# Optimization experiments

Hardware: AMD Instinct MI355X
Metric: run time of the kernel (lower is better)

The kernel has to match this reference:

```python
import jax, jax.numpy as jnp
import numpy as np

B, S, D, H, M, E, K = 4, 2048, 1024, 2048, 64, 8, 2  # batch, seq, d_model, max_neurons, moe_hidden, experts, top_k


def setup_inputs() -> dict:
    key = jax.random.key(0)
    ks = jax.random.split(key, 10)
    r = lambda k, shape: jax.random.normal(k, shape, dtype=jnp.float32) * 0.02
    return {
        "inputs_embeds": jax.random.normal(ks[0], (B, S, D), dtype=jnp.float32),
        "enc_W": r(ks[1], (D, H)), "enc_b": jnp.zeros((H,), jnp.float32),
        "s2c_W": r(ks[2], (H, M)), "s2c_b": jnp.zeros((M,), jnp.float32),
        "rW1": r(ks[3], (M, 64)), "rb1": jnp.zeros((64,), jnp.float32),
        "rW2": r(ks[4], (64, E)), "rb2": jnp.zeros((E,), jnp.float32),
        "We1": r(ks[5], (E, M, H // 2)), "be1": jnp.zeros((E, H // 2), jnp.float32),
        "We2": r(ks[6], (E, H // 2, M)), "be2": jnp.zeros((E, M), jnp.float32),
        "c2s_W": r(ks[7], (M, H)), "c2s_b": jnp.zeros((H,), jnp.float32),
        "dec_W": r(ks[8], (H, D)), "dec_b": jnp.zeros((D,), jnp.float32),
        "ln_g": jnp.ones((D,), jnp.float32), "ln_b": jnp.zeros((D,), jnp.float32),
    }


def _layernorm(x, g, b, eps=1e-5):
    mu = x.mean(-1, keepdims=True)
    var = ((x - mu) ** 2).mean(-1, keepdims=True)
    return (x - mu) * jax.lax.rsqrt(var + eps) * g + b


def _forward(inputs_embeds, enc_W, enc_b, s2c_W, s2c_b, rW1, rb1, rW2, rb2,
             We1, be1, We2, be2, c2s_W, c2s_b, dec_W, dec_b, ln_g, ln_b):
    b, s, _ = inputs_embeds.shape
    # GIFNeuron encoder (rate-coded surrogate spikes)
    spikes_enc = jax.nn.sigmoid(inputs_embeds @ enc_W + enc_b)          # (B,S,H)
    flat = spikes_enc.reshape(b * s, H)                                  # (N,H)
    # SpikeToContinuousBridge ('rate'): projection to MoE hidden
    cont = flat @ s2c_W + s2c_b                                          # (N,M)
    # LiquidMoERouter: 2-layer router, softmax, top-k, renormalize
    logits = jnp.tanh(cont @ rW1 + rb1) @ rW2 + rb2                      # (N,E)
    probs = jax.nn.softmax(logits, axis=-1)
    topw, topi = jax.lax.top_k(probs, K)                                 # (N,K)
    w = topw / topw.sum(-1, keepdims=True)
    # dense per-token per-expert gate == sum_k weights[:,k] * (indices[:,k]==e)
    gates = (jax.nn.one_hot(topi, E, dtype=cont.dtype) * w[..., None]).sum(1)  # (N,E)
    # SNNExpert MLP per expert, dense dispatch + weighted combine (index_add equivalent)
    h = jax.nn.relu(jnp.einsum('nm,emh->enh', cont, We1) + be1[:, None, :])    # (E,N,H/2)
    expert_out = jnp.einsum('enh,ehm->enm', h, We2) + be2[:, None, :]          # (E,N,M)
    output_flat = jnp.einsum('enm,ne->nm', expert_out, gates)                  # (N,M)
    # ContinuousToSpikeBridge ('poisson', expected rate), 2D -> 1 timestep
    spikes_moe = jax.nn.sigmoid(output_flat @ c2s_W + c2s_b).reshape(b, s, H)
    # GIFNeuron decoder + LayerNorm
    decoded = jax.nn.sigmoid(spikes_moe @ dec_W + dec_b)                 # (B,S,D)
    return _layernorm(decoded, ln_g, ln_b)


def reference(inputs_embeds, enc_W, enc_b, s2c_W, s2c_b, rW1, rb1, rW2, rb2,
              We1, be1, We2, be2, c2s_W, c2s_b, dec_W, dec_b, ln_g, ln_b):
    return _forward(inputs_embeds, enc_W, enc_b, s2c_W, s2c_b, rW1, rb1, rW2, rb2,
                    We1, be1, We2, be2, c2s_W, c2s_b, dec_W, dec_b, ln_g, ln_b)
```

## Files before the change

### kernel.cpp

```cpp
#include <hip/hip_runtime.h>
#include <hip/hip_bf16.h>
#include <cstdint>
#include <cstddef>

#define TOK    8192
#define DMODEL 1024
#define HDIM   2048
#define MDIM   64
#define NEXP   8
#define HHALF  1024

using f32x4  = __attribute__((ext_vector_type(4))) float;
using bf16x8 = __attribute__((ext_vector_type(8))) __bf16;
using bf16x4 = __attribute__((ext_vector_type(4))) __bf16;

__device__ __forceinline__ void async16(const void* g, void* l) {
  __builtin_amdgcn_global_load_lds(
      (const __attribute__((address_space(1))) unsigned int*)g,
      (__attribute__((address_space(3))) unsigned int*)l, 16, 0, 0);
}

__global__ __launch_bounds__(256) void preamble_kernel(
    const float* __restrict__ X, __bf16* __restrict__ Xb,
    const float* __restrict__ encW, __bf16* __restrict__ encWT,
    const float* __restrict__ s2cW, __bf16* __restrict__ s2cWT,
    const float* __restrict__ c2sW, __bf16* __restrict__ c2sWT,
    const float* __restrict__ decW, __bf16* __restrict__ decWT,
    const float* __restrict__ We1, __bf16* __restrict__ We1T,
    const float* __restrict__ We2, __bf16* __restrict__ We2T) {
  __shared__ float ts[32][33];
  const int tid = threadIdx.x;
  int b = blockIdx.x;
  if (b < 8192) {
    int i = b * 256 + tid;
    float4 v = ((const float4*)X)[i];
    bf16x4 o = { (__bf16)v.x, (__bf16)v.y, (__bf16)v.z, (__bf16)v.w };
    ((bf16x4*)Xb)[i] = o;
    return;
  }
  b -= 8192;
  const float* in; __bf16* outp; int R, C, tx, ty;
  if (b < 2048)              { in = encW; outp = encWT; R = 1024; C = 2048; tx = b % 64; ty = b / 64; }
  else if ((b -= 2048) < 128){ in = s2cW; outp = s2cWT; R = 2048; C = 64;   tx = b % 2;  ty = b / 2;  }
  else if ((b -= 128) < 128) { in = c2sW; outp = c2sWT; R = 64;   C = 2048; tx = b % 64; ty = b / 64; }
  else if ((b -= 128) < 2048){ in = decW; outp = decWT; R = 2048; C = 1024; tx = b % 32; ty = b / 32; }
  else if ((b -= 2048) < 512){ int s = b / 64, t = b % 64;
                               in = We1 + (size_t)s * 65536; outp = We1T + (size_t)s * 65536;
                               R = 64; C = 1024; tx = t % 32; ty = t / 32; }
  else                       { b -= 512; int s = b / 64, t = b % 64;
                               in = We2 + (size_t)s * 65536; outp = We2T + (size_t)s * 65536;
                               R = 1024; C = 64; tx = t % 2; ty = t / 2; }
  const int c0 = tx * 32, r0 = ty * 32;
  const int x = tid & 31, y = tid >> 5;
  #pragma unroll
  for (int i = y; i < 32; i += 8) ts[i][x] = in[(size_t)(r0 + i) * C + c0 + x];
  __syncthreads();
  #pragma unroll
  for (int i = y; i < 32; i += 8)
    outp[(size_t)(c0 + i) * R + r0 + x] = (__bf16)ts[x][i];
}
#define PREAMBLE_BLOCKS (8192 + 2048 + 128 + 128 + 2048 + 512 + 512)

template <int BN, int WAVES, int NBUF, int OUT_BF16, int ACT, int BIAS>
__global__ __launch_bounds__(WAVES * 64, WAVES == 8 ? 2 : 1) void gemm_mt(
    const __bf16* __restrict__ A, const __bf16* __restrict__ Bt,
    const float* __restrict__ bias, void* __restrict__ Cout,
    int M, int N, int K) {
  constexpr int BM = 256, BK = 64;
  constexpr int A_ISSUES = BM / (8 * WAVES);
  constexpr int B_ISSUES = BN / (8 * WAVES);
  constexpr int LOADS = A_ISSUES + B_ISSUES;
  static_assert((NBUF == 2 && LOADS == 8) || (NBUF == 3 && LOADS == 12),
                "vmcnt literals assume LOADS=8 (NBUF2) or 12 (NBUF3)");
  __shared__ __bf16 As[NBUF * BM * BK];
  __shared__ __bf16 Bs[NBUF * BN * BK];
  const int tid = threadIdx.x;
  const int wave = tid >> 6, lane = tid & 63;
  const int quad = lane >> 4, l16 = lane & 15;
  const int m0 = blockIdx.x * BM, n0 = blockIdx.y * BN;
  const int wm = (wave & 1) * 128;
  const int wn = (wave >> 1) * 64;
  const int lrow = lane >> 3, lchunk = lane & 7;
  f32x4 acc[8][4] = {};

  const __bf16* aSrc[A_ISSUES];
  const __bf16* bSrc[B_ISSUES];
  #pragma unroll
  for (int t = 0; t < A_ISSUES; ++t) {
    int row = (t * WAVES + wave) * 8 + lrow;
    aSrc[t] = A + (size_t)(m0 + row) * K + (lchunk ^ (row & 7)) * 8;
  }
  #pragma unroll
  for (int t = 0; t < B_ISSUES; ++t) {
    int row = (t * WAVES + wave) * 8 + lrow;
    bSrc[t] = Bt + (size_t)(n0 + row) * K + (lchunk ^ (row & 7)) * 8;
  }
  int aOff[8], bOff[4];
  #pragma unroll
  for (int rf = 0; rf < 8; ++rf) {
    int row = wm + rf * 16 + l16;
    aOff[rf] = row * BK + ((quad ^ (row & 7)) * 8);
  }
  #pragma unroll
  for (int cf = 0; cf < 4; ++cf) {
    int row = wn + cf * 16 + l16;
    bOff[cf] = row * BK + ((quad ^ (row & 7)) * 8);
  }

  auto stage = [&](__bf16* Ad, __bf16* Bd) {
    #pragma unroll
    for (int t = 0; t < A_ISSUES; ++t) {
      async16(aSrc[t], Ad + (t * WAVES + wave) * 8 * BK);
      aSrc[t] += BK;
    }
    #pragma unroll
    for (int t = 0; t < B_ISSUES; ++t) {
      async16(bSrc[t], Bd + (t * WAVES + wave) * 8 * BK);
      bSrc[t] += BK;
    }
  };

  __bf16 *cA0 = As, *cA1 = As + BM * BK, *cA2 = As + 2 * BM * BK;
  __bf16 *cB0 = Bs, *cB1 = Bs + BN * BK, *cB2 = Bs + 2 * BN * BK;
  const int nt = K / BK;
  stage(cA0, cB0);
  if constexpr (NBUF == 3) stage(cA1, cB1);

  for (int t = 0; t < nt; ++t) {
    if constexpr (NBUF == 2) {
      if (t + 1 < nt) stage(cA1, cB1);
    } else {
      if (t + 2 < nt) stage(cA2, cB2);
    }
    const int ahead = nt - 1 - t;
    if constexpr (NBUF == 2) {
      if (ahead >= 1) asm volatile("s_waitcnt vmcnt(8)" ::: "memory");
      else            asm volatile("s_waitcnt vmcnt(0)" ::: "memory");
    } else {
      if (ahead >= 2)      asm volatile("s_waitcnt vmcnt(24)" ::: "memory");
      else if (ahead == 1) asm volatile("s_waitcnt vmcnt(12)" ::: "memory");
      else                 asm volatile("s_waitcnt vmcnt(0)" ::: "memory");
    }
    asm volatile("s_barrier" ::: "memory");

    bf16x8 af[4], ag[4], bv[4], bw[4];
    #pragma unroll
    for (int r = 0; r < 4; ++r) af[r] = *(const bf16x8*)(cA0 + aOff[r]);
    #pragma unroll
    for (int c = 0; c < 4; ++c) bv[c] = *(const bf16x8*)(cB0 + bOff[c]);
    #pragma unroll
    for (int r = 0; r < 4; ++r) ag[r] = *(const bf16x8*)(cA0 + aOff[4 + r]);
    __builtin_amdgcn_s_setprio(1);
    #pragma unroll
    for (int c = 0; c < 4; ++c)
      #pragma unroll
      for (int r = 0; r < 4; ++r)
        acc[r][c] = __builtin_amdgcn_mfma_f32_16x16x32_bf16(af[r], bv[c], acc[r][c], 0, 0, 0);
    __builtin_amdgcn_s_setprio(0);
    asm volatile("s_barrier" ::: "memory");
    #pragma unroll
    for (int r = 0; r < 4; ++r) af[r] = *(const bf16x8*)(cA0 + (aOff[r] ^ 32));
    #pragma unroll
    for (int c = 0; c < 4; ++c) bw[c] = *(const bf16x8*)(cB0 + (bOff[c] ^ 32));
    __builtin_amdgcn_s_setprio(1);
    #pragma unroll
    for (int c = 0; c < 4; ++c)
      #pragma unroll
      for (int r = 0; r < 4; ++r)
        acc[4 + r][c] = __builtin_amdgcn_mfma_f32_16x16x32_bf16(ag[r], bv[c], acc[4 + r][c], 0, 0, 0);
    __builtin_amdgcn_s_setprio(0);
    asm volatile("s_barrier" ::: "memory");
    #pragma unroll
    for (int r = 0; r < 4; ++r) ag[r] = *(const bf16x8*)(cA0 + (aOff[4 + r] ^ 32));
    __builtin_amdgcn_s_setprio(1);
    #pragma unroll
    for (int c = 0; c < 4; ++c)
      #pragma unroll
      for (int r = 0; r < 4; ++r)
        acc[r][c] = __builtin_amdgcn_mfma_f32_16x16x32_bf16(af[r], bw[c], acc[r][c], 0, 0, 0);
    __builtin_amdgcn_s_setprio(0);
    asm volatile("s_barrier" ::: "memory");
    __builtin_amdgcn_s_setprio(1);
    #pragma unroll
    for (int c = 0; c < 4; ++c)
      #pragma unroll
      for (int r = 0; r < 4; ++r)
        acc[4 + r][c] = __builtin_amdgcn_mfma_f32_16x16x32_bf16(ag[r], bw[c], acc[4 + r][c], 0, 0, 0);
    __builtin_amdgcn_s_setprio(0);
    asm volatile("s_barrier" ::: "memory");

    if constexpr (NBUF == 2) {
      __bf16* x;
      x = cA0; cA0 = cA1; cA1 = x;
      x = cB0; cB0 = cB1; cB1 = x;
    } else {
      __bf16* x;
      x = cA0; cA0 = cA1; cA1 = cA2; cA2 = x;
      x = cB0; cB0 = cB1; cB1 = cB2; cB2 = x;
    }
  }

  #pragma unroll
  for (int rf = 0; rf < 8; ++rf)
    #pragma unroll
    for (int cf = 0; cf < 4; ++cf)
      #pragma unroll
      for (int r = 0; r < 4; ++r) {
        int m = m0 + wm + rf * 16 + quad * 4 + r;
        int n = n0 + wn + cf * 16 + l16;
        float v = acc[rf][cf][r];
        if (BIAS) v += bias[n];
        if (ACT == 1) v = 1.0f / (1.0f + __expf(-v));
        if (OUT_BF16)
          ((__bf16*)Cout)[(size_t)m * N + n] = (__bf16)v;
        else
          ((float*)Cout)[(size_t)m * N + n] = v;
      }
}

template <int BM, int BN, int WAVES, int OUT_BF16, int ACT, int BIAS, int SUMA>
__global__ __launch_bounds__(WAVES * 64) void gemm_bt(
    const __bf16* __restrict__ A, const __bf16* __restrict__ Bt,
    const float* __restrict__ bias, void* __restrict__ Cout,
    int M, int N, int K, const __bf16* __restrict__ A2) {
  constexpr int BK = 64;
  constexpr int WAVES_N = WAVES / 2;
  constexpr int WTM = BM / 32;
  constexpr int WTN = BN / (WAVES_N * 16);
  constexpr int NBUF = SUMA ? 1 : 3;
  constexpr int A_ISSUES = BM / (8 * WAVES);
  constexpr int B_ISSUES = BN / (8 * WAVES);
  static_assert(SUMA || (A_ISSUES + B_ISSUES == 6), "vmcnt literal assumes 6 loads/stage");
  __shared__ __bf16 As[NBUF * BM * BK];
  __shared__ __bf16 Bs[NBUF * BN * BK];
  const int tid = threadIdx.x;
  const int wave = tid >> 6, lane = tid & 63;
  const int quad = lane >> 4, l16 = lane & 15;
  const int m0 = blockIdx.x * BM, n0 = blockIdx.y * BN;
  const int ks = K / gridDim.z;
  const int kbeg = blockIdx.z * ks;
  const int wm = (wave & 1) * (BM / 2);
  const int wn = (wave >> 1) * (BN / WAVES_N);
  const int lrow = lane >> 3;
  const int lchunk = lane & 7;
  f32x4 acc[WTM][WTN] = {};

  const __bf16* aSrc[A_ISSUES];
  const __bf16* bSrc[B_ISSUES];
  #pragma unroll
  for (int t = 0; t < A_ISSUES; ++t) {
    int row = (t * WAVES + wave) * 8 + lrow;
    aSrc[t] = A + (size_t)(m0 + row) * K + kbeg + (lchunk ^ (row & 7)) * 8;
  }
  #pragma unroll
  for (int t = 0; t < B_ISSUES; ++t) {
    int row = (t * WAVES + wave) * 8 + lrow;
    bSrc[t] = Bt + (size_t)(n0 + row) * K + kbeg + (lchunk ^ (row & 7)) * 8;
  }
  int aOff[WTM][2], bOff[WTN][2];
  #pragma unroll
  for (int i = 0; i < WTM; ++i) {
    int row = wm + i * 16 + l16;
    #pragma unroll
    for (int kk = 0; kk < 2; ++kk)
      aOff[i][kk] = row * BK + (((kk * 4 + quad) ^ (row & 7)) * 8);
  }
  #pragma unroll
  for (int j = 0; j < WTN; ++j) {
    int row = wn + j * 16 + l16;
    #pragma unroll
    for (int kk = 0; kk < 2; ++kk)
      bOff[j][kk] = row * BK + (((kk * 4 + quad) ^ (row & 7)) * 8);
  }

  auto stage = [&](__bf16* Ad, __bf16* Bd) {
    #pragma unroll
    for (int t = 0; t < A_ISSUES; ++t) {
      async16(aSrc[t], Ad + (t * WAVES + wave) * 8 * BK);
      aSrc[t] += BK;
    }
    #pragma unroll
    for (int t = 0; t < B_ISSUES; ++t) {
      async16(bSrc[t], Bd + (t * WAVES + wave) * 8 * BK);
      bSrc[t] += BK;
    }
  };
  auto compute = [&](const __bf16* Ab, const __bf16* Bb) {
    #pragma unroll
    for (int kk = 0; kk < 2; ++kk) {
      bf16x8 af[WTM], bfr[WTN];
      #pragma unroll
      for (int i = 0; i < WTM; ++i) af[i] = *(const bf16x8*)(Ab + aOff[i][kk]);
      #pragma unroll
      for (int j = 0; j < WTN; ++j) bfr[j] = *(const bf16x8*)(Bb + bOff[j][kk]);
      #pragma unroll
      for (int i = 0; i < WTM; ++i)
        #pragma unroll
        for (int j = 0; j < WTN; ++j)
          acc[i][j] = __builtin_amdgcn_mfma_f32_16x16x32_bf16(af[i], bfr[j], acc[i][j], 0, 0, 0);
    }
  };

  const int niter = ks / BK;
  if constexpr (SUMA) {
    for (int it = 0; it < niter; ++it) {
      __syncthreads();
      #pragma unroll
      for (int t = 0; t < A_ISSUES; ++t) {
        int row = (t * WAVES + wave) * 8 + lrow;
        size_t go = (size_t)(m0 + row) * K + kbeg + it * BK + lchunk * 8;
        bf16x8 a0 = *(const bf16x8*)(A + go);
        bf16x8 a1 = *(const bf16x8*)(A2 + go);
        bf16x8 s;
        #pragma unroll
        for (int q = 0; q < 8; ++q) s[q] = (__bf16)((float)a0[q] + (float)a1[q]);
        *(bf16x8*)(As + row * BK + ((lchunk ^ (row & 7)) * 8)) = s;
      }
      #pragma unroll
      for (int t = 0; t < B_ISSUES; ++t) {
        async16(bSrc[t], Bs + (t * WAVES + wave) * 8 * BK);
        bSrc[t] += BK;
      }
      __syncthreads();
      compute(As, Bs);
    }
  } else {
    __bf16* a0 = As;  __bf16* a1 = As + BM * BK;  __bf16* a2 = As + 2 * BM * BK;
    __bf16* b0 = Bs;  __bf16* b1 = Bs + BN * BK;  __bf16* b2 = Bs + 2 * BN * BK;
    stage(a0, b0);
    if (niter > 1) stage(a1, b1);
    for (int it = 0; it < niter; ++it) {
      if (it + 1 < niter) asm volatile("s_waitcnt vmcnt(6)" ::: "memory");
      else                asm volatile("s_waitcnt vmcnt(0)" ::: "memory");
      __builtin_amdgcn_s_barrier();
      if (it + 2 < niter) stage(a2, b2);
      compute(a0, b0);
      __bf16* t;
      t = a0; a0 = a1; a1 = a2; a2 = t;
      t = b0; b0 = b1; b1 = b2; b2 = t;
    }
  }

  char* Cz = (char*)Cout + (size_t)blockIdx.z * M * N * (OUT_BF16 ? 2 : 4);
  #pragma unroll
  for (int i = 0; i < WTM; ++i)
    #pragma unroll
    for (int j = 0; j < WTN; ++j)
      #pragma unroll
      for (int r = 0; r < 4; ++r) {
        int m = m0 + wm + i * 16 + quad * 4 + r;
        int n = n0 + wn + j * 16 + l16;
        float v = acc[i][j][r];
        if (BIAS) v += bias[n];
        if (ACT == 1) v = 1.0f / (1.0f + __expf(-v));
        if (OUT_BF16)
          ((__bf16*)Cz)[(size_t)m * N + n] = (__bf16)v;
        else
          ((float*)Cz)[(size_t)m * N + n] = v;
      }
}

__global__ __launch_bounds__(256) void router_kernel(
    const float* __restrict__ contP, const float* __restrict__ s2c_b,
    const float* __restrict__ rW1, const float* __restrict__ rb1,
    const float* __restrict__ rW2, const float* __restrict__ rb2,
    __bf16* __restrict__ contB, int* __restrict__ e01,
    float2* __restrict__ g01) {
  const int wave = threadIdx.x >> 6, lane = threadIdx.x & 63;
  const int n = blockIdx.x * 4 + wave;
  const size_t base = (size_t)n * 64 + lane;
  const size_t slab = (size_t)TOK * 64;
  float c = contP[base] + contP[base + slab] + contP[base + 2 * slab] +
            contP[base + 3 * slab] + s2c_b[lane];
  contB[base] = (__bf16)c;
  float acc = rb1[lane];
  #pragma unroll
  for (int i = 0; i < 64; ++i) {
    float ci = __shfl(c, i);
    acc = fmaf(ci, rW1[i * 64 + lane], acc);
  }
  float t = tanhf(acc);
  float logit[8];
  #pragma unroll
  for (int e = 0; e < 8; ++e) {
    float v = t * rW2[lane * 8 + e];
    #pragma unroll
    for (int o = 32; o; o >>= 1) v += __shfl_xor(v, o);
    logit[e] = v + rb2[e];
  }
  float mx = logit[0];
  #pragma unroll
  for (int e = 1; e < 8; ++e) mx = fmaxf(mx, logit[e]);
  float p[8];
  #pragma unroll
  for (int e = 0; e < 8; ++e) p[e] = __expf(logit[e] - mx);
  float v0 = p[0]; int e0 = 0;
  #pragma unroll
  for (int e = 1; e < 8; ++e) if (p[e] > v0) { v0 = p[e]; e0 = e; }
  float v1 = -1.0f; int e1 = 0;
  #pragma unroll
  for (int e = 0; e < 8; ++e) if (e != e0 && p[e] > v1) { v1 = p[e]; e1 = e; }
  float inv = 1.0f / (v0 + v1);
  if (lane == 0) {
    e01[n] = e0 | (e1 << 8);
    g01[n] = make_float2(v0 * inv, v1 * inv);
  }
}

__global__ __launch_bounds__(256) void moe_fused_kernel(
    const __bf16* __restrict__ contB, const __bf16* __restrict__ We1T,
    const __bf16* __restrict__ We2T, const float* __restrict__ be1,
    const float* __restrict__ be2, const int* __restrict__ e01,
    const float2* __restrict__ g01, __bf16* __restrict__ slab0,
    __bf16* __restrict__ slab1) {
  constexpr int TT = 128;
  const int e = blockIdx.y;
  const int t0 = blockIdx.x * TT;
  __shared__ __bf16 cont_s[TT * 64];
  __shared__ __bf16 w1_s[64 * 64];
  __shared__ __bf16 w2_s[64 * 64];
  __shared__ __bf16 h_s[TT * 64];
  __shared__ int   e01_s[TT];
  __shared__ float g0_s[TT], g1_s[TT];
  const int tid = threadIdx.x;
  const int wave = tid >> 6, lane = tid & 63;
  const int quad = lane >> 4, l16 = lane & 15;
  if (tid < TT) {
    e01_s[tid] = e01[t0 + tid];
    float2 g = g01[t0 + tid];
    g0_s[tid] = g.x; g1_s[tid] = g.y;
  }
  for (int i = tid; i < TT * 8; i += 256) {
    int r = i >> 3, cc = i & 7;
    *(uint4*)(cont_s + r * 64 + ((cc ^ (r & 7)) * 8)) =
        *(const uint4*)(contB + (size_t)(t0 + r) * 64 + cc * 8);
  }
  const int wtok = wave * 32;
  f32x4 acc2[2][4] = {};
  for (int hc = 0; hc < HHALF; hc += 64) {
    __syncthreads();
    for (int c = tid; c < 512; c += 256) {
      int r = c >> 3, cc = c & 7;
      *(uint4*)(w1_s + r * 64 + ((cc ^ (r & 7)) * 8)) =
          *(const uint4*)(We1T + ((size_t)e * HHALF + hc + r) * 64 + cc * 8);
      *(uint4*)(w2_s + r * 64 + ((cc ^ (r & 7)) * 8)) =
          *(const uint4*)(We2T + ((size_t)e * 64 + r) * HHALF + hc + cc * 8);
    }
    __syncthreads();
    f32x4 acc1[2][4] = {};
    #pragma unroll
    for (int kk = 0; kk < 2; ++kk) {
      bf16x8 af[2], bfr[4];
      #pragma unroll
      for (int i = 0; i < 2; ++i) {
        int row = wtok + i * 16 + l16;
        af[i] = *(const bf16x8*)(cont_s + row * 64 + (((kk * 4 + quad) ^ (row & 7)) * 8));
      }
      #pragma unroll
      for (int j = 0; j < 4; ++j) {
        int row = j * 16 + l16;
        bfr[j] = *(const bf16x8*)(w1_s + row * 64 + (((kk * 4 + quad) ^ (row & 7)) * 8));
      }
      #pragma unroll
      for (int i = 0; i < 2; ++i)
        #pragma unroll
        for (int j = 0; j < 4; ++j)
          acc1[i][j] = __builtin_amdgcn_mfma_f32_16x16x32_bf16(af[i], bfr[j], acc1[i][j], 0, 0, 0);
    }
    #pragma unroll
    for (int i = 0; i < 2; ++i)
      #pragma unroll
      for (int j = 0; j < 4; ++j)
        #pragma unroll
        for (int r = 0; r < 4; ++r) {
          int tr = wtok + i * 16 + quad * 4 + r;
          int hcol = j * 16 + l16;
          float v = acc1[i][j][r] + be1[e * HHALF + hc + hcol];
          h_s[tr * 64 + (((hcol >> 3) ^ (tr & 7)) * 8) + (hcol & 7)] =
              (__bf16)fmaxf(v, 0.0f);
        }
    #pragma unroll
    for (int kk = 0; kk < 2; ++kk) {
      bf16x8 af[2], bfr[4];
      #pragma unroll
      for (int i = 0; i < 2; ++i) {
        int row = wtok + i * 16 + l16;
        af[i] = *(const bf16x8*)(h_s + row * 64 + (((kk * 4 + quad) ^ (row & 7)) * 8));
      }
      #pragma unroll
      for (int j = 0; j < 4; ++j) {
        int row = j * 16 + l16;
        bfr[j] = *(const bf16x8*)(w2_s + row * 64 + (((kk * 4 + quad) ^ (row & 7)) * 8));
      }
      #pragma unroll
      for (int i = 0; i < 2; ++i)
        #pragma unroll
        for (int j = 0; j < 4; ++j)
          acc2[i][j] = __builtin_amdgcn_mfma_f32_16x16x32_bf16(af[i], bfr[j], acc2[i][j], 0, 0, 0);
    }
  }
  #pragma unroll
  for (int i = 0; i < 2; ++i)
    #pragma unroll
    for (int j = 0; j < 4; ++j)
      #pragma unroll
      for (int r = 0; r < 4; ++r) {
        int tr = wtok + i * 16 + quad * 4 + r;
        int m = j * 16 + l16;
        int pe = e01_s[tr];
        size_t o = (size_t)(t0 + tr) * 64 + m;
        if ((pe & 0xff) == e)
          slab0[o] = (__bf16)(g0_s[tr] * (acc2[i][j][r] + be2[e * 64 + m]));
        else if (((pe >> 8) & 0xff) == e)
          slab1[o] = (__bf16)(g1_s[tr] * (acc2[i][j][r] + be2[e * 64 + m]));
      }
}

__global__ __launch_bounds__(256) void ln_kernel(
    const float* __restrict__ x, const float* __restrict__ g,
    const float* __restrict__ b, float* __restrict__ out) {
  const int row = blockIdx.x;
  const float4 v = ((const float4*)(x + (size_t)row * 1024))[threadIdx.x];
  float s1 = v.x + v.y + v.z + v.w;
  float s2 = v.x * v.x + v.y * v.y + v.z * v.z + v.w * v.w;
  #pragma unroll
  for (int o = 32; o; o >>= 1) { s1 += __shfl_xor(s1, o); s2 += __shfl_xor(s2, o); }
  __shared__ float ws1[4], ws2[4];
  const int wave = threadIdx.x >> 6, lane = threadIdx.x & 63;
  if (lane == 0) { ws1[wave] = s1; ws2[wave] = s2; }
  __syncthreads();
  s1 = ws1[0] + ws1[1] + ws1[2] + ws1[3];
  s2 = ws2[0] + ws2[1] + ws2[2] + ws2[3];
  const float mu = s1 * (1.0f / 1024.0f);
  const float var = s2 * (1.0f / 1024.0f) - mu * mu;
  const float inv = rsqrtf(var + 1e-5f);
  const int col = threadIdx.x * 4;
  const float4 gv = *(const float4*)(g + col);
  const float4 bv = *(const float4*)(b + col);
  float4 o;
  o.x = (v.x - mu) * inv * gv.x + bv.x;
  o.y = (v.y - mu) * inv * gv.y + bv.y;
  o.z = (v.z - mu) * inv * gv.z + bv.z;
  o.w = (v.w - mu) * inv * gv.w + bv.w;
  *(float4*)(out + (size_t)row * 1024 + col) = o;
}

extern "C" void kernel_launch(void* const* d_in, const int* in_sizes, int n_in,
                              void* d_out, int out_size, void* d_ws, size_t ws_size,
                              hipStream_t stream) {
  const float* X     = (const float*)d_in[0];
  const float* enc_W = (const float*)d_in[1];
  const float* enc_b = (const float*)d_in[2];
  const float* s2c_W = (const float*)d_in[3];
  const float* s2c_b = (const float*)d_in[4];
  const float* rW1   = (const float*)d_in[5];
  const float* rb1   = (const float*)d_in[6];
  const float* rW2   = (const float*)d_in[7];
  const float* rb2   = (const float*)d_in[8];
  const float* We1   = (const float*)d_in[9];
  const float* be1   = (const float*)d_in[10];
  const float* We2   = (const float*)d_in[11];
  const float* be2   = (const float*)d_in[12];
  const float* c2s_W = (const float*)d_in[13];
  const float* c2s_b = (const float*)d_in[14];
  const float* dec_W = (const float*)d_in[15];
  const float* dec_b = (const float*)d_in[16];
  const float* ln_g  = (const float*)d_in[17];
  const float* ln_b  = (const float*)d_in[18];
  float* out = (float*)d_out;

  char* ws = (char*)d_ws;
  size_t off = 0;
  auto take = [&](size_t bytes) -> char* {
    char* p = ws + off;
    off = (off + bytes + 255) & ~(size_t)255;
    return p;
  };
  const size_t SLAB = (size_t)TOK * HDIM * 2;
  char*   slabA     = take(SLAB);
  char*   slabB     = take(SLAB);
  __bf16* encWT     = (__bf16*)take((size_t)HDIM * DMODEL * 2);
  __bf16* s2cWT     = (__bf16*)take((size_t)MDIM * HDIM * 2);
  __bf16* c2sWT     = (__bf16*)take((size_t)HDIM * MDIM * 2);
  __bf16* decWT     = (__bf16*)take((size_t)DMODEL * HDIM * 2);
  __bf16* We1T      = (__bf16*)take((size_t)NEXP * HHALF * MDIM * 2);
  __bf16* We2T      = (__bf16*)take((size_t)NEXP * MDIM * HHALF * 2);
  __bf16* contB     = (__bf16*)take((size_t)TOK * MDIM * 2);
  int*    e01       = (int*)take((size_t)TOK * 4);
  float2* g01       = (float2*)take((size_t)TOK * 8);
  __bf16* oslab0    = (__bf16*)take((size_t)TOK * MDIM * 2);
  __bf16* oslab1    = (__bf16*)take((size_t)TOK * MDIM * 2);
  if (off > ws_size) return;

  __bf16* Xb        = (__bf16*)slabA;
  float*  contP     = (float*)(slabA + (size_t)TOK * DMODEL * 2);
  __bf16* spikesMoe = (__bf16*)slabA;
  __bf16* spikesEnc = (__bf16*)slabB;
  float*  decoded   = (float*)slabB;

  preamble_kernel<<<PREAMBLE_BLOCKS, 256, 0, stream>>>(
      X, Xb, enc_W, encWT, s2c_W, s2cWT, c2s_W, c2sWT, dec_W, decWT,
      We1, We1T, We2, We2T);

  gemm_mt<256, 8, 2, 1, 1, 1><<<dim3(TOK / 256, HDIM / 256), 512, 0, stream>>>(
      Xb, encWT, enc_b, spikesEnc, TOK, HDIM, DMODEL);
  gemm_bt<128, 64, 4, 0, 0, 0, 0><<<dim3(TOK / 128, 1, 4), 256, 0, stream>>>(
      spikesEnc, s2cWT, nullptr, contP, TOK, MDIM, HDIM, nullptr);
  router_kernel<<<TOK / 4, 256, 0, stream>>>(contP, s2c_b, rW1, rb1, rW2, rb2,
                                             contB, e01, g01);
  moe_fused_kernel<<<dim3(TOK / 128, NEXP), 256, 0, stream>>>(
      contB, We1T, We2T, be1, be2, e01, g01, oslab0, oslab1);
  gemm_bt<128, 128, 4, 1, 1, 1, 1><<<dim3(TOK / 128, HDIM / 128, 1), 256, 0, stream>>>(
      oslab0, c2sWT, c2s_b, spikesMoe, TOK, HDIM, MDIM, oslab1);
  gemm_mt<128, 4, 3, 0, 1, 1><<<dim3(TOK / 256, DMODEL / 128), 256, 0, stream>>>(
      spikesMoe, decWT, dec_b, decoded, TOK, DMODEL, HDIM);
  ln_kernel<<<TOK, 256, 0, stream>>>(decoded, ln_g, ln_b, out);
}
```

Before: 320.3 us.

## Switch MoE to sparse top-k dispatch and rework GEMM pipelining

New measurement: 311.7 us. -2.7%, faster.

```diff
diff --git a/kernel.cpp b/kernel.cpp
--- a/kernel.cpp
+++ b/kernel.cpp
@@ -62,7 +62,7 @@
 #define PREAMBLE_BLOCKS (8192 + 2048 + 128 + 128 + 2048 + 512 + 512)
 
 template <int BN, int WAVES, int NBUF, int OUT_BF16, int ACT, int BIAS>
-__global__ __launch_bounds__(WAVES * 64, WAVES == 8 ? 2 : 1) void gemm_mt(
+__global__ __launch_bounds__(WAVES * 64, 2) void gemm_mt(
     const __bf16* __restrict__ A, const __bf16* __restrict__ Bt,
     const float* __restrict__ bias, void* __restrict__ Cout,
     int M, int N, int K) {
@@ -70,8 +70,7 @@
   constexpr int A_ISSUES = BM / (8 * WAVES);
   constexpr int B_ISSUES = BN / (8 * WAVES);
   constexpr int LOADS = A_ISSUES + B_ISSUES;
-  static_assert((NBUF == 2 && LOADS == 8) || (NBUF == 3 && LOADS == 12),
-                "vmcnt literals assume LOADS=8 (NBUF2) or 12 (NBUF3)");
+  static_assert(NBUF == 2 && LOADS == 8, "vmcnt literal assumes LOADS=8");
   __shared__ __bf16 As[NBUF * BM * BK];
   __shared__ __bf16 Bs[NBUF * BN * BK];
   const int tid = threadIdx.x;
@@ -120,27 +119,15 @@
     }
   };
 
-  __bf16 *cA0 = As, *cA1 = As + BM * BK, *cA2 = As + 2 * BM * BK;
-  __bf16 *cB0 = Bs, *cB1 = Bs + BN * BK, *cB2 = Bs + 2 * BN * BK;
+  __bf16 *cA0 = As, *cA1 = As + BM * BK;
+  __bf16 *cB0 = Bs, *cB1 = Bs + BN * BK;
   const int nt = K / BK;
   stage(cA0, cB0);
-  if constexpr (NBUF == 3) stage(cA1, cB1);
 
   for (int t = 0; t < nt; ++t) {
-    if constexpr (NBUF == 2) {
-      if (t + 1 < nt) stage(cA1, cB1);
-    } else {
-      if (t + 2 < nt) stage(cA2, cB2);
-    }
-    const int ahead = nt - 1 - t;
-    if constexpr (NBUF == 2) {
-      if (ahead >= 1) asm volatile("s_waitcnt vmcnt(8)" ::: "memory");
-      else            asm volatile("s_waitcnt vmcnt(0)" ::: "memory");
-    } else {
-      if (ahead >= 2)      asm volatile("s_waitcnt vmcnt(24)" ::: "memory");
-      else if (ahead == 1) asm volatile("s_waitcnt vmcnt(12)" ::: "memory");
-      else                 asm volatile("s_waitcnt vmcnt(0)" ::: "memory");
-    }
+    if (t + 1 < nt) stage(cA1, cB1);
+    if (t + 1 < nt) asm volatile("s_waitcnt vmcnt(8)" ::: "memory");
+    else            asm volatile("s_waitcnt vmcnt(0)" ::: "memory");
     asm volatile("s_barrier" ::: "memory");
 
     bf16x8 af[4], ag[4], bv[4], bw[4];
@@ -189,15 +176,9 @@
     __builtin_amdgcn_s_setprio(0);
     asm volatile("s_barrier" ::: "memory");
 
-    if constexpr (NBUF == 2) {
-      __bf16* x;
-      x = cA0; cA0 = cA1; cA1 = x;
-      x = cB0; cB0 = cB1; cB1 = x;
-    } else {
-      __bf16* x;
-      x = cA0; cA0 = cA1; cA1 = cA2; cA2 = x;
-      x = cB0; cB0 = cB1; cB1 = cB2; cB2 = x;
-    }
+    __bf16* x;
+    x = cA0; cA0 = cA1; cA1 = x;
+    x = cB0; cB0 = cB1; cB1 = x;
   }
 
   #pragma unroll
@@ -227,10 +208,9 @@
   constexpr int WAVES_N = WAVES / 2;
   constexpr int WTM = BM / 32;
   constexpr int WTN = BN / (WAVES_N * 16);
-  constexpr int NBUF = SUMA ? 1 : 3;
+  constexpr int NBUF = SUMA ? 1 : 2;
   constexpr int A_ISSUES = BM / (8 * WAVES);
   constexpr int B_ISSUES = BN / (8 * WAVES);
-  static_assert(SUMA || (A_ISSUES + B_ISSUES == 6), "vmcnt literal assumes 6 loads/stage");
   __shared__ __bf16 As[NBUF * BM * BK];
   __shared__ __bf16 Bs[NBUF * BN * BK];
   const int tid = threadIdx.x;
@@ -325,20 +305,20 @@
       compute(As, Bs);
     }
   } else {
-    __bf16* a0 = As;  __bf16* a1 = As + BM * BK;  __bf16* a2 = As + 2 * BM * BK;
-    __bf16* b0 = Bs;  __bf16* b1 = Bs + BN * BK;  __bf16* b2 = Bs + 2 * BN * BK;
-    stage(a0, b0);
-    if (niter > 1) stage(a1, b1);
-    for (int it = 0; it < niter; ++it) {
-      if (it + 1 < niter) asm volatile("s_waitcnt vmcnt(6)" ::: "memory");
-      else                asm volatile("s_waitcnt vmcnt(0)" ::: "memory");
+    __bf16* curA = As;  __bf16* nxtA = As + BM * BK;
+    __bf16* curB = Bs;  __bf16* nxtB = Bs + BN * BK;
+    stage(curA, curB);
+    asm volatile("s_waitcnt vmcnt(0)" ::: "memory");
+    __builtin_amdgcn_s_barrier();
+    for (int it = 0; it < niter - 1; ++it) {
+      stage(nxtA, nxtB);
+      compute(curA, curB);
+      asm volatile("s_waitcnt vmcnt(0)" ::: "memory");
       __builtin_amdgcn_s_barrier();
-      if (it + 2 < niter) stage(a2, b2);
-      compute(a0, b0);
-      __bf16* t;
-      t = a0; a0 = a1; a1 = a2; a2 = t;
-      t = b0; b0 = b1; b1 = b2; b2 = t;
-    }
+      { __bf16* t = curA; curA = nxtA; nxtA = t; }
+      { __bf16* t = curB; curB = nxtB; nxtB = t; }
+    }
+    compute(curA, curB);
   }
 
   char* Cz = (char*)Cout + (size_t)blockIdx.z * M * N * (OUT_BF16 ? 2 : 4);
@@ -365,7 +345,8 @@
     const float* __restrict__ rW1, const float* __restrict__ rb1,
     const float* __restrict__ rW2, const float* __restrict__ rb2,
     __bf16* __restrict__ contB, int* __restrict__ e01,
-    float2* __restrict__ g01) {
+    float2* __restrict__ g01, int* __restrict__ cnt) {
+  if (blockIdx.x == 0 && threadIdx.x < NEXP) cnt[threadIdx.x] = 0;
   const int wave = threadIdx.x >> 6, lane = threadIdx.x & 63;
   const int n = blockIdx.x * 4 + wave;
   const size_t base = (size_t)n * 64 + lane;
@@ -407,36 +388,62 @@
   }
 }
 
-__global__ __launch_bounds__(256) void moe_fused_kernel(
+__global__ __launch_bounds__(256) void fill_kernel(
+    const int* __restrict__ e01, int* __restrict__ cnt,
+    unsigned* __restrict__ idxb) {
+  __shared__ int lcnt[NEXP], lbase[NEXP];
+  const int tid = threadIdx.x;
+  if (tid < NEXP) lcnt[tid] = 0;
+  __syncthreads();
+  const int n = blockIdx.x * 256 + tid;
+  const int pe = e01[n];
+  const int e0 = pe & 0xff, e1 = (pe >> 8) & 0xff;
+  const int p0 = atomicAdd(&lcnt[e0], 1);
+  const int p1 = atomicAdd(&lcnt[e1], 1);
+  __syncthreads();
+  if (tid < NEXP) lbase[tid] = atomicAdd(&cnt[tid], lcnt[tid]);
+  __syncthreads();
+  idxb[e0 * TOK + lbase[e0] + p0] = (unsigned)n;
+  idxb[e1 * TOK + lbase[e1] + p1] = (unsigned)n | 0x80000000u;
+}
+
+__global__ __launch_bounds__(256) void moe_sparse_kernel(
     const __bf16* __restrict__ contB, const __bf16* __restrict__ We1T,
     const __bf16* __restrict__ We2T, const float* __restrict__ be1,
-    const float* __restrict__ be2, const int* __restrict__ e01,
-    const float2* __restrict__ g01, __bf16* __restrict__ slab0,
-    __bf16* __restrict__ slab1) {
-  constexpr int TT = 128;
+    const float* __restrict__ be2, const unsigned* __restrict__ idxb,
+    const int* __restrict__ cnt, const float2* __restrict__ g01,
+    __bf16* __restrict__ slab0, __bf16* __restrict__ slab1) {
+  constexpr int TT = 64;
   const int e = blockIdx.y;
-  const int t0 = blockIdx.x * TT;
+  const int start = blockIdx.x * TT;
+  const int ne = cnt[e];
+  if (start >= ne) return;
+  const int nval = min(TT, ne - start);
   __shared__ __bf16 cont_s[TT * 64];
   __shared__ __bf16 w1_s[64 * 64];
   __shared__ __bf16 w2_s[64 * 64];
   __shared__ __bf16 h_s[TT * 64];
-  __shared__ int   e01_s[TT];
-  __shared__ float g0_s[TT], g1_s[TT];
+  __shared__ unsigned tok_s[TT];
+  __shared__ float gate_s[TT];
   const int tid = threadIdx.x;
   const int wave = tid >> 6, lane = tid & 63;
   const int quad = lane >> 4, l16 = lane & 15;
   if (tid < TT) {
-    e01_s[tid] = e01[t0 + tid];
-    float2 g = g01[t0 + tid];
-    g0_s[tid] = g.x; g1_s[tid] = g.y;
-  }
+    unsigned v = idxb[e * TOK + start + ((tid < nval) ? tid : 0)];
+    unsigned tok = v & 0x7fffffffu;
+    float2 g = g01[tok];
+    tok_s[tid] = v;
+    gate_s[tid] = (v >> 31) ? g.y : g.x;
+  }
+  __syncthreads();
   for (int i = tid; i < TT * 8; i += 256) {
     int r = i >> 3, cc = i & 7;
+    unsigned tok = tok_s[r] & 0x7fffffffu;
     *(uint4*)(cont_s + r * 64 + ((cc ^ (r & 7)) * 8)) =
-        *(const uint4*)(contB + (size_t)(t0 + r) * 64 + cc * 8);
-  }
-  const int wtok = wave * 32;
-  f32x4 acc2[2][4] = {};
+        *(const uint4*)(contB + (size_t)tok * 64 + cc * 8);
+  }
+  const int wtok = wave * 16;
+  f32x4 acc2[4] = {};
   for (int hc = 0; hc < HHALF; hc += 64) {
     __syncthreads();
     for (int c = tid; c < 512; c += 256) {
@@ -447,14 +454,13 @@
           *(const uint4*)(We2T + ((size_t)e * 64 + r) * HHALF + hc + cc * 8);
     }
     __syncthreads();
-    f32x4 acc1[2][4] = {};
+    f32x4 acc1[4] = {};
     #pragma unroll
     for (int kk = 0; kk < 2; ++kk) {
-      bf16x8 af[2], bfr[4];
-      #pragma unroll
-      for (int i = 0; i < 2; ++i) {
-        int row = wtok + i * 16 + l16;
-        af[i] = *(const bf16x8*)(cont_s + row * 64 + (((kk * 4 + quad) ^ (row & 7)) * 8));
+      bf16x8 af, bfr[4];
+      {
+        int row = wtok + l16;
+        af = *(const bf16x8*)(cont_s + row * 64 + (((kk * 4 + quad) ^ (row & 7)) * 8));
       }
       #pragma unroll
       for (int j = 0; j < 4; ++j) {
@@ -462,30 +468,25 @@
         bfr[j] = *(const bf16x8*)(w1_s + row * 64 + (((kk * 4 + quad) ^ (row & 7)) * 8));
       }
       #pragma unroll
-      for (int i = 0; i < 2; ++i)
-        #pragma unroll
-        for (int j = 0; j < 4; ++j)
-          acc1[i][j] = __builtin_amdgcn_mfma_f32_16x16x32_bf16(af[i], bfr[j], acc1[i][j], 0, 0, 0);
-    }
-    #pragma unroll
-    for (int i = 0; i < 2; ++i)
-      #pragma unroll
       for (int j = 0; j < 4; ++j)
-        #pragma unroll
-        for (int r = 0; r < 4; ++r) {
-          int tr = wtok + i * 16 + quad * 4 + r;
-          int hcol = j * 16 + l16;
-          float v = acc1[i][j][r] + be1[e * HHALF + hc + hcol];
-          h_s[tr * 64 + (((hcol >> 3) ^ (tr & 7)) * 8) + (hcol & 7)] =
-              (__bf16)fmaxf(v, 0.0f);
-        }
+        acc1[j] = __builtin_amdgcn_mfma_f32_16x16x32_bf16(af, bfr[j], acc1[j], 0, 0, 0);
+    }
+    #pragma unroll
+    for (int j = 0; j < 4; ++j)
+      #pragma unroll
+      for (int r = 0; r < 4; ++r) {
+        int tr = wtok + quad * 4 + r;
+        int hcol = j * 16 + l16;
+        float v = acc1[j][r] + be1[e * HHALF + hc + hcol];
+        h_s[tr * 64 + (((hcol >> 3) ^ (tr & 7)) * 8) + (hcol & 7)] =
+            (__bf16)fmaxf(v, 0.0f);
+      }
     #pragma unroll
     for (int kk = 0; kk < 2; ++kk) {
-      bf16x8 af[2], bfr[4];
-      #pragma unroll
-      for (int i = 0; i < 2; ++i) {
-        int row = wtok + i * 16 + l16;
-        af[i] = *(const bf16x8*)(h_s + row * 64 + (((kk * 4 + quad) ^ (row & 7)) * 8));
+      bf16x8 af, bfr[4];
+      {
+        int row = wtok + l16;
+        af = *(const bf16x8*)(h_s + row * 64 + (((kk * 4 + quad) ^ (row & 7)) * 8));
       }
       #pragma unroll
       for (int j = 0; j < 4; ++j) {
@@ -493,27 +494,24 @@
         bfr[j] = *(const bf16x8*)(w2_s + row * 64 + (((kk * 4 + quad) ^ (row & 7)) * 8));
       }
       #pragma unroll
-      for (int i = 0; i < 2; ++i)
-        #pragma unroll
-        for (int j = 0; j < 4; ++j)
-          acc2[i][j] = __builtin_amdgcn_mfma_f32_16x16x32_bf16(af[i], bfr[j], acc2[i][j], 0, 0, 0);
-    }
-  }
-  #pragma unroll
-  for (int i = 0; i < 2; ++i)
-    #pragma unroll
-    for (int j = 0; j < 4; ++j)
-      #pragma unroll
-      for (int r = 0; r < 4; ++r) {
-        int tr = wtok + i * 16 + quad * 4 + r;
+      for (int j = 0; j < 4; ++j)
+        acc2[j] = __builtin_amdgcn_mfma_f32_16x16x32_bf16(af, bfr[j], acc2[j], 0, 0, 0);
+    }
+  }
+  #pragma unroll
+  for (int j = 0; j < 4; ++j)
+    #pragma unroll
+    for (int r = 0; r < 4; ++r) {
+      int tr = wtok + quad * 4 + r;
+      if (tr < nval) {
+        unsigned v = tok_s[tr];
+        unsigned tok = v & 0x7fffffffu;
         int m = j * 16 + l16;
-        int pe = e01_s[tr];
-        size_t o = (size_t)(t0 + tr) * 64 + m;
-        if ((pe & 0xff) == e)
-          slab0[o] = (__bf16)(g0_s[tr] * (acc2[i][j][r] + be2[e * 64 + m]));
-        else if (((pe >> 8) & 0xff) == e)
-          slab1[o] = (__bf16)(g1_s[tr] * (acc2[i][j][r] + be2[e * 64 + m]));
-      }
+        float o = gate_s[tr] * (acc2[j][r] + be2[e * 64 + m]);
+        __bf16* slab = (v >> 31) ? slab1 : slab0;
+        slab[(size_t)tok * 64 + m] = (__bf16)o;
+      }
+    }
 }
 
 __global__ __launch_bounds__(256) void ln_kernel(
@@ -590,6 +588,8 @@
   float2* g01       = (float2*)take((size_t)TOK * 8);
   __bf16* oslab0    = (__bf16*)take((size_t)TOK * MDIM * 2);
   __bf16* oslab1    = (__bf16*)take((size_t)TOK * MDIM * 2);
+  int*     cnt      = (int*)take((size_t)NEXP * 4);
+  unsigned* idxb    = (unsigned*)take((size_t)NEXP * TOK * 4);
   if (off > ws_size) return;
 
   __bf16* Xb        = (__bf16*)slabA;
@@ -607,12 +607,13 @@
   gemm_bt<128, 64, 4, 0, 0, 0, 0><<<dim3(TOK / 128, 1, 4), 256, 0, stream>>>(
       spikesEnc, s2cWT, nullptr, contP, TOK, MDIM, HDIM, nullptr);
   router_kernel<<<TOK / 4, 256, 0, stream>>>(contP, s2c_b, rW1, rb1, rW2, rb2,
-                                             contB, e01, g01);
-  moe_fused_kernel<<<dim3(TOK / 128, NEXP), 256, 0, stream>>>(
-      contB, We1T, We2T, be1, be2, e01, g01, oslab0, oslab1);
+                                             contB, e01, g01, cnt);
+  fill_kernel<<<TOK / 256, 256, 0, stream>>>(e01, cnt, idxb);
+  moe_sparse_kernel<<<dim3(TOK / 64, NEXP), 256, 0, stream>>>(
+      contB, We1T, We2T, be1, be2, idxb, cnt, g01, oslab0, oslab1);
   gemm_bt<128, 128, 4, 1, 1, 1, 1><<<dim3(TOK / 128, HDIM / 128, 1), 256, 0, stream>>>(
       oslab0, c2sWT, c2s_b, spikesMoe, TOK, HDIM, MDIM, oslab1);
-  gemm_mt<128, 4, 3, 0, 1, 1><<<dim3(TOK / 256, DMODEL / 128), 256, 0, stream>>>(
-      spikesMoe, decWT, dec_b, decoded, TOK, DMODEL, HDIM);
+  gemm_bt<128, 128, 4, 0, 1, 1, 0><<<dim3(TOK / 128, DMODEL / 128, 1), 256, 0, stream>>>(
+      spikesMoe, decWT, dec_b, decoded, TOK, DMODEL, HDIM, nullptr);
   ln_kernel<<<TOK, 256, 0, stream>>>(decoded, ln_g, ln_b, out);
 }
```
